# Performance work log

Measured on AMD Instinct MI355X. Metric: run time of the kernel, lower is better.

The kernel has to match this reference:

```python
import jax, jax.numpy as jnp
import numpy as np

BETA = 0.25  # commitment loss weight


def setup_inputs() -> dict:
    key = jax.random.key(0)
    k1, k2 = jax.random.split(key)
    N, K, d = 131072, 1024, 64
    z_e = jax.random.normal(k1, (N, d), dtype=jnp.float32)
    scale = 1.0 / np.sqrt(d)
    codebook = jax.random.uniform(k2, (K, d), minval=-scale, maxval=scale, dtype=jnp.float32)
    return {"z_e": z_e, "codebook": codebook}


def reference(z_e, codebook):
    d = codebook.shape[-1]
    flat = z_e.reshape(-1, d)                                  # (N, d)
    z_sq = jnp.sum(flat ** 2, axis=-1, keepdims=True)          # (N, 1)
    c_sq = jnp.sum(codebook ** 2, axis=-1)[None, :]            # (1, K)
    zc = flat @ codebook.T                                     # (N, K)
    dists = z_sq - 2.0 * zc + c_sq
    idx_flat = jnp.argmin(dists, axis=-1)                      # (N,)
    e_flat = codebook[idx_flat]                                # (N, d)
    z_q_flat_st = flat + jax.lax.stop_gradient(e_flat - flat)  # straight-through
    codebook_loss = jnp.mean((e_flat - jax.lax.stop_gradient(flat)) ** 2)
    commitment_loss = jnp.mean((jax.lax.stop_gradient(e_flat) - flat) ** 2)
    vq_loss = codebook_loss + BETA * commitment_loss
    indices = idx_flat.reshape(z_e.shape[:-1])
    z_q_st = z_q_flat_st.reshape(z_e.shape)
    return (indices, z_q_st, vq_loss)
```

## Files before the change

### kernel.cpp

```cpp
#include <hip/hip_runtime.h>
#include <stdint.h>

#define DIM 64
#define KC 1024
#define TILE 64
#define NT (KC / TILE)
#define TAU_HALF 5.0e-4f
#define FLAG_CAP 16384

typedef float f32x4 __attribute__((ext_vector_type(4)));
typedef short short8 __attribute__((ext_vector_type(8)));

__device__ __forceinline__ unsigned short bf16_rn(float f) {
  union { float f; uint32_t u; } v; v.f = f;
  uint32_t u = v.u;
  uint32_t r = u + 0x7fffu + ((u >> 16) & 1u);
  return (unsigned short)(r >> 16);
}
__device__ __forceinline__ float bf16_f32(unsigned short h) {
  union { uint32_t u; float f; } v; v.u = ((uint32_t)h) << 16;
  return v.f;
}
__device__ __forceinline__ void gll16(const void* g, void* l) {
  __builtin_amdgcn_global_load_lds(
      (const __attribute__((address_space(1))) void*)g,
      (__attribute__((address_space(3))) void*)l, 16, 0, 0);
}

__global__ void k1_prep(const float* __restrict__ cb,
                        unsigned short* __restrict__ cb_hi,
                        unsigned short* __restrict__ cb_lo,
                        float* __restrict__ csqh,
                        int* __restrict__ cnt) {
  const int k = blockIdx.x, j = threadIdx.x;
  const float c = cb[k * DIM + j];
  const unsigned short hi = bf16_rn(c);
  const float hif = bf16_f32(hi);
  const unsigned short lo = bf16_rn(c - hif);
  cb_hi[k * DIM + j] = hi;
  cb_lo[k * DIM + j] = lo;
  float s = c * c;
  #pragma unroll
  for (int off = 32; off >= 1; off >>= 1) s += __shfl_xor(s, off);
  if (j == 0) csqh[k] = -0.5f * s;
  if (k == 0 && j == 0) *cnt = 0;
}

__launch_bounds__(256, 4)
__global__ void k2_argmin(const float* __restrict__ z,
                          const unsigned short* __restrict__ cb_hi,
                          const unsigned short* __restrict__ cb_lo,
                          const float* __restrict__ csqh,
                          float* __restrict__ out_idx,
                          int* __restrict__ cnt,
                          int* __restrict__ flags,
                          float* __restrict__ partials) {
  __shared__ unsigned short lds_cb[2 * 8192];
  __shared__ float lds_csq[KC];

  const int tid  = threadIdx.x;
  const int lane = tid & 63;
  const int wv   = tid >> 6;
  const int wr   = wv >> 1;
  const int wc   = wv & 1;
  const int lg   = lane >> 4;
  const int lr   = lane & 15;
  const int row0 = blockIdx.x * 128;

  const unsigned short* gsrc[4];
  #pragma unroll
  for (int p = 0; p < 4; ++p) {
    const int cl = (p & 1) * 32 + wv * 8 + (lane >> 3);
    const int ch = (lane & 7) ^ (cl & 7);
    gsrc[p] = ((p >> 1) ? cb_lo : cb_hi) + cl * DIM + ch * 8;
  }

#define STAGE(tt, bs)                                                         \
  {                                                                           \
    const int _toff = (tt) * (TILE * DIM);                                    \
    _Pragma("unroll")                                                         \
    for (int p = 0; p < 4; ++p) {                                             \
      gll16(gsrc[p] + _toff,                                                  \
            (char*)lds_cb + (bs) * 16384 + (p * 256 + wv * 64) * 16);         \
    }                                                                         \
  }

  STAGE(0, 0);
  ((f32x4*)lds_csq)[tid] = ((const f32x4*)csqh)[tid];

  short8 zhi[4][2], zlo[4][2];
  float zsq[4];
  #pragma unroll
  for (int rt = 0; rt < 4; ++rt) {
    const int row = row0 + wr * 64 + rt * 16 + lr;
    float sq = 0.0f;
    #pragma unroll
    for (int ks = 0; ks < 2; ++ks) {
      const float* p = z + row * DIM + ks * 32 + lg * 8;
      const f32x4 va = *(const f32x4*)p;
      const f32x4 vb = *(const f32x4*)(p + 4);
      sq = fmaf(va[0], va[0], sq); sq = fmaf(va[1], va[1], sq);
      sq = fmaf(va[2], va[2], sq); sq = fmaf(va[3], va[3], sq);
      sq = fmaf(vb[0], vb[0], sq); sq = fmaf(vb[1], vb[1], sq);
      sq = fmaf(vb[2], vb[2], sq); sq = fmaf(vb[3], vb[3], sq);
      union { uint32_t w[4]; short8 s8; } H, L;
      #pragma unroll
      for (int pr = 0; pr < 4; ++pr) {
        const float f0 = (pr < 2) ? va[2 * pr]     : vb[2 * pr - 4];
        const float f1 = (pr < 2) ? va[2 * pr + 1] : vb[2 * pr - 3];
        const uint32_t u0 = __float_as_uint(f0);
        const uint32_t u1 = __float_as_uint(f1);
        H.w[pr] = __builtin_amdgcn_perm(u1, u0, 0x07060302u);
        const float l0 = f0 - __uint_as_float(u0 & 0xffff0000u);
        const float l1 = f1 - __uint_as_float(u1 & 0xffff0000u);
        uint32_t lw;
        asm("v_cvt_pk_bf16_f32 %0, %1, %2" : "=v"(lw) : "v"(l0), "v"(l1));
        L.w[pr] = lw;
      }
      zhi[rt][ks] = H.s8;
      zlo[rt][ks] = L.s8;
    }
    zsq[rt] = sq;
  }

  float M1[4], M2[4];
  int I1[4];
  #pragma unroll
  for (int rt = 0; rt < 4; ++rt) { M1[rt] = -3.0e38f; M2[rt] = -3.0e38f; I1[rt] = 0; }

  __syncthreads();

  for (int t = 0; t < NT; ++t) {
    if (t < NT - 1) STAGE(t + 1, (t + 1) & 1);
    const char* bufb = (const char*)lds_cb + (t & 1) * 16384;
    #pragma unroll
    for (int ct = 0; ct < 2; ++ct) {
      const int cbase = t * TILE + wc * 32 + ct * 16 + lg * 4;
      const f32x4 init = *(const f32x4*)&lds_csq[cbase];
      const int cl2 = wc * 32 + ct * 16 + lr;
      short8 cf[2][2];
      #pragma unroll
      for (int sp = 0; sp < 2; ++sp) {
        #pragma unroll
        for (int ks = 0; ks < 2; ++ks) {
          const int off = sp * 8192 + cl2 * 128 + (((ks * 4 + lg) ^ (cl2 & 7)) * 16);
          cf[sp][ks] = *(const short8*)(bufb + off);
        }
      }
      #pragma unroll
      for (int rt = 0; rt < 4; ++rt) {
        f32x4 acc = init;
        acc = __builtin_amdgcn_mfma_f32_16x16x32_bf16(cf[0][0], zhi[rt][0], acc, 0, 0, 0);
        acc = __builtin_amdgcn_mfma_f32_16x16x32_bf16(cf[0][1], zhi[rt][1], acc, 0, 0, 0);
        acc = __builtin_amdgcn_mfma_f32_16x16x32_bf16(cf[0][0], zlo[rt][0], acc, 0, 0, 0);
        acc = __builtin_amdgcn_mfma_f32_16x16x32_bf16(cf[0][1], zlo[rt][1], acc, 0, 0, 0);
        acc = __builtin_amdgcn_mfma_f32_16x16x32_bf16(cf[1][0], zhi[rt][0], acc, 0, 0, 0);
        acc = __builtin_amdgcn_mfma_f32_16x16x32_bf16(cf[1][1], zhi[rt][1], acc, 0, 0, 0);
        #pragma unroll
        for (int j = 0; j < 4; ++j) {
          const float s = acc[j];
          M2[rt] = __builtin_amdgcn_fmed3f(s, M1[rt], M2[rt]);
          const bool take = s > M1[rt];
          M1[rt] = fmaxf(s, M1[rt]);
          I1[rt] = take ? (cbase + j) : I1[rt];
        }
      }
    }
    __syncthreads();
  }

  float* S  = (float*)lds_cb;
  float* S2 = S + 256;
  int*   SI = (int*)(S + 512);
  float* ZS = (float*)(SI + 256);
  float* CT = ZS + 128;

  #pragma unroll
  for (int rt = 0; rt < 4; ++rt) {
    float m1 = M1[rt], m2 = M2[rt];
    int i1 = I1[rt];
    #pragma unroll
    for (int off = 16; off <= 32; off <<= 1) {
      const float o1 = __shfl_xor(m1, off);
      const float o2 = __shfl_xor(m2, off);
      const int   oi = __shfl_xor(i1, off);
      m2 = fmaxf(fmaxf(m2, o2), fminf(m1, o1));
      const bool take = (o1 > m1) || (o1 == m1 && oi < i1);
      if (take) { m1 = o1; i1 = oi; }
    }
    float zq = zsq[rt];
    zq += __shfl_xor(zq, 16);
    zq += __shfl_xor(zq, 32);
    if (lg == 0) {
      const int r = wr * 64 + rt * 16 + lr;
      S[wc * 128 + r]  = m1;
      S2[wc * 128 + r] = m2;
      SI[wc * 128 + r] = i1;
      if (wc == 0) ZS[r] = zq;
    }
  }
  __syncthreads();
  if (tid < 128) {
    const float a1 = S[tid],  b1 = S[128 + tid];
    const float a2 = S2[tid], b2 = S2[128 + tid];
    const int   ai = SI[tid], bi = SI[128 + tid];
    const bool takeB = (b1 > a1) || (b1 == a1 && bi < ai);
    const float m1 = takeB ? b1 : a1;
    const int  idx = takeB ? bi : ai;
    const float m2 = fmaxf(fmaxf(a2, b2), fminf(a1, b1));
    const int row = row0 + tid;
    out_idx[row] = (float)idx;
    CT[tid] = ZS[tid] - 2.0f * m1;
    if (m1 - m2 < TAU_HALF) {
      const int p = atomicAdd(cnt, 1);
      if (p < FLAG_CAP) flags[p] = row;
    }
  }
  __syncthreads();
  if (tid < 64) {
    float c = CT[tid] + CT[tid + 64];
    #pragma unroll
    for (int off = 32; off >= 1; off >>= 1) c += __shfl_xor(c, off);
    if (tid == 0) partials[blockIdx.x] = c;
  }
#undef STAGE
}

__global__ void k3_rescue(const float* __restrict__ z,
                          const float* __restrict__ cb,
                          const float* __restrict__ csqh,
                          float* __restrict__ out_idx,
                          const int* __restrict__ cnt,
                          const int* __restrict__ flags) {
  int n = *cnt;
  if (n > FLAG_CAP) n = FLAG_CAP;
  const int lane = threadIdx.x & 63;
  const int w = blockIdx.x * 4 + (threadIdx.x >> 6);
  for (int i = w; i < n; i += gridDim.x * 4) {
    const int row = flags[i];
    const f32x4* zr4 = (const f32x4*)(z + (size_t)row * DIM);
    float m1 = -3.0e38f;
    int i1 = 0;
    for (int kk = 0; kk < 16; ++kk) {
      const int k = lane * 16 + kk;
      const f32x4* cp = (const f32x4*)(cb + (size_t)k * DIM);
      float acc = csqh[k];
      #pragma unroll
      for (int j4 = 0; j4 < DIM / 4; ++j4) {
        const f32x4 c4 = cp[j4];
        const f32x4 z4 = zr4[j4];
        acc = fmaf(z4[0], c4[0], acc);
        acc = fmaf(z4[1], c4[1], acc);
        acc = fmaf(z4[2], c4[2], acc);
        acc = fmaf(z4[3], c4[3], acc);
      }
      if (acc > m1) { m1 = acc; i1 = k; }
    }
    #pragma unroll
    for (int off = 32; off >= 1; off >>= 1) {
      const float o1 = __shfl_xor(m1, off);
      const int   oi = __shfl_xor(i1, off);
      if (o1 > m1 || (o1 == m1 && oi < i1)) { m1 = o1; i1 = oi; }
    }
    if (lane == 0) out_idx[row] = (float)i1;
  }
}

__global__ void k4_scatter(const float* __restrict__ cb,
                           const float* __restrict__ out_idx,
                           float* __restrict__ zq) {
  const int gid = blockIdx.x * 256 + threadIdx.x;
  const int row = gid >> 2;
  const int q0  = (gid & 3) * 4;
  const int idx = (int)out_idx[row];
  const f32x4* src = (const f32x4*)(cb + (size_t)idx * DIM) + q0;
  f32x4* dst = (f32x4*)(zq + (size_t)row * DIM) + q0;
  dst[0] = src[0]; dst[1] = src[1]; dst[2] = src[2]; dst[3] = src[3];
}

__global__ void k5_reduce(const float* __restrict__ partials,
                          float* __restrict__ loss_slot,
                          float scale, int nb) {
  __shared__ float wsum[4];
  const int tid = threadIdx.x;
  float s = 0.0f;
  for (int i = tid; i < nb / 4; i += 256) {
    const f32x4 v = ((const f32x4*)partials)[i];
    s += (v[0] + v[1]) + (v[2] + v[3]);
  }
  #pragma unroll
  for (int off = 32; off >= 1; off >>= 1) s += __shfl_xor(s, off);
  if ((tid & 63) == 0) wsum[tid >> 6] = s;
  __syncthreads();
  if (tid == 0) *loss_slot = (wsum[0] + wsum[1] + wsum[2] + wsum[3]) * scale;
}

extern "C" void kernel_launch(void* const* d_in, const int* in_sizes, int n_in,
                              void* d_out, int out_size, void* d_ws, size_t ws_size,
                              hipStream_t stream) {
  const float* z  = (const float*)d_in[0];
  const float* cb = (const float*)d_in[1];
  const int N = in_sizes[0] / DIM;

  float* out       = (float*)d_out;
  float* out_idx   = out;
  float* zq        = out + N;
  float* loss_slot = out + N + (size_t)N * DIM;

  unsigned short* cb_hi = (unsigned short*)d_ws;
  unsigned short* cb_lo = cb_hi + KC * DIM;
  float* csqh = (float*)(cb_lo + KC * DIM);
  int* cnt    = (int*)(csqh + KC);
  int* flags  = cnt + 64;
  float* partials = (float*)(flags + FLAG_CAP);

  const int nb2 = N / 128;
  const float scale = 1.25f / ((float)N * (float)DIM);

  k1_prep<<<KC, DIM, 0, stream>>>(cb, cb_hi, cb_lo, csqh, cnt);
  k2_argmin<<<nb2, 256, 0, stream>>>(z, cb_hi, cb_lo, csqh, out_idx, cnt, flags, partials);
  k3_rescue<<<256, 256, 0, stream>>>(z, cb, csqh, out_idx, cnt, flags);
  k4_scatter<<<N / 64, 256, 0, stream>>>(cb, out_idx, zq);
  k5_reduce<<<1, 256, 0, stream>>>(partials, loss_slot, scale, nb2);
}
```

Baseline: 185.5 us.

## Hold full bf16 codebook in LDS, drop lo split, fuse scatter into argmin

Loads the whole codebook, as bf16 hi parts only, into LDS once per 1024-thread block of 512 rows, replacing the double-buffered tiled staging. It drops the codebook lo-part MFMAs (four MFMAs per tile instead of six) and widens the near-tie rescue threshold to compensate for the lower precision. The z_q gather is fused into the argmin and rescue kernels, which removes the separate scatter kernel. The risks are more rows flagged for the scalar rescue pass, whose flag capacity is raised, and lower occupancy from the 128KB+ LDS allocation.

```diff
diff --git a/kernel.cpp b/kernel.cpp
--- a/kernel.cpp
+++ b/kernel.cpp
@@ -3,10 +3,9 @@
 
 #define DIM 64
 #define KC 1024
-#define TILE 64
-#define NT (KC / TILE)
-#define TAU_HALF 5.0e-4f
-#define FLAG_CAP 16384
+#define ROWS_PER_BLOCK 512
+#define TAU 8.0e-3f
+#define FLAG_CAP 65536
 
 typedef float f32x4 __attribute__((ext_vector_type(4)));
 typedef short short8 __attribute__((ext_vector_type(8)));
@@ -17,10 +16,6 @@
   uint32_t r = u + 0x7fffu + ((u >> 16) & 1u);
   return (unsigned short)(r >> 16);
 }
-__device__ __forceinline__ float bf16_f32(unsigned short h) {
-  union { uint32_t u; float f; } v; v.u = ((uint32_t)h) << 16;
-  return v.f;
-}
 __device__ __forceinline__ void gll16(const void* g, void* l) {
   __builtin_amdgcn_global_load_lds(
       (const __attribute__((address_space(1))) void*)g,
@@ -29,16 +24,11 @@
 
 __global__ void k1_prep(const float* __restrict__ cb,
                         unsigned short* __restrict__ cb_hi,
-                        unsigned short* __restrict__ cb_lo,
                         float* __restrict__ csqh,
                         int* __restrict__ cnt) {
   const int k = blockIdx.x, j = threadIdx.x;
   const float c = cb[k * DIM + j];
-  const unsigned short hi = bf16_rn(c);
-  const float hif = bf16_f32(hi);
-  const unsigned short lo = bf16_rn(c - hif);
-  cb_hi[k * DIM + j] = hi;
-  cb_lo[k * DIM + j] = lo;
+  cb_hi[k * DIM + j] = bf16_rn(c);
   float s = c * c;
   #pragma unroll
   for (int off = 32; off >= 1; off >>= 1) s += __shfl_xor(s, off);
@@ -46,57 +36,45 @@
   if (k == 0 && j == 0) *cnt = 0;
 }
 
-__launch_bounds__(256, 4)
+__launch_bounds__(1024, 4)
 __global__ void k2_argmin(const float* __restrict__ z,
                           const unsigned short* __restrict__ cb_hi,
-                          const unsigned short* __restrict__ cb_lo,
                           const float* __restrict__ csqh,
+                          const float* __restrict__ cb,
                           float* __restrict__ out_idx,
+                          float* __restrict__ zq,
                           int* __restrict__ cnt,
                           int* __restrict__ flags,
                           float* __restrict__ partials) {
-  __shared__ unsigned short lds_cb[2 * 8192];
+  __shared__ unsigned short lds_cb[KC * DIM];
   __shared__ float lds_csq[KC];
+  __shared__ float wpart[16];
 
   const int tid  = threadIdx.x;
   const int lane = tid & 63;
   const int wv   = tid >> 6;
-  const int wr   = wv >> 1;
-  const int wc   = wv & 1;
   const int lg   = lane >> 4;
   const int lr   = lane & 15;
-  const int row0 = blockIdx.x * 128;
-
-  const unsigned short* gsrc[4];
-  #pragma unroll
-  for (int p = 0; p < 4; ++p) {
-    const int cl = (p & 1) * 32 + wv * 8 + (lane >> 3);
-    const int ch = (lane & 7) ^ (cl & 7);
-    gsrc[p] = ((p >> 1) ? cb_lo : cb_hi) + cl * DIM + ch * 8;
-  }
-
-#define STAGE(tt, bs)                                                         \
-  {                                                                           \
-    const int _toff = (tt) * (TILE * DIM);                                    \
-    _Pragma("unroll")                                                         \
-    for (int p = 0; p < 4; ++p) {                                             \
-      gll16(gsrc[p] + _toff,                                                  \
-            (char*)lds_cb + (bs) * 16384 + (p * 256 + wv * 64) * 16);         \
-    }                                                                         \
-  }
-
-  STAGE(0, 0);
-  ((f32x4*)lds_csq)[tid] = ((const f32x4*)csqh)[tid];
-
-  short8 zhi[4][2], zlo[4][2];
-  float zsq[4];
-  #pragma unroll
-  for (int rt = 0; rt < 4; ++rt) {
-    const int row = row0 + wr * 64 + rt * 16 + lr;
+  const int row0 = blockIdx.x * ROWS_PER_BLOCK;
+
+  #pragma unroll
+  for (int p = 0; p < 8; ++p) {
+    const int linear = p * 1024 + tid;
+    const int ch = linear & 7;
+    const int cl = linear >> 3;
+    gll16(cb_hi + cl * DIM + ((ch ^ (cl & 7)) * 8), (char*)lds_cb + linear * 16);
+  }
+  if (tid < KC / 4) ((f32x4*)lds_csq)[tid] = ((const f32x4*)csqh)[tid];
+
+  short8 zhi[2][2], zlo[2][2];
+  float zsq[2];
+  #pragma unroll
+  for (int rt = 0; rt < 2; ++rt) {
+    const int row = row0 + wv * 32 + rt * 16 + lr;
     float sq = 0.0f;
     #pragma unroll
     for (int ks = 0; ks < 2; ++ks) {
-      const float* p = z + row * DIM + ks * 32 + lg * 8;
+      const float* p = z + (size_t)row * DIM + ks * 32 + lg * 8;
       const f32x4 va = *(const f32x4*)p;
       const f32x4 vb = *(const f32x4*)(p + 4);
       sq = fmaf(va[0], va[0], sq); sq = fmaf(va[1], va[1], sq);
@@ -123,60 +101,43 @@
     zsq[rt] = sq;
   }
 
-  float M1[4], M2[4];
-  int I1[4];
-  #pragma unroll
-  for (int rt = 0; rt < 4; ++rt) { M1[rt] = -3.0e38f; M2[rt] = -3.0e38f; I1[rt] = 0; }
-
-  __syncthreads();
-
-  for (int t = 0; t < NT; ++t) {
-    if (t < NT - 1) STAGE(t + 1, (t + 1) & 1);
-    const char* bufb = (const char*)lds_cb + (t & 1) * 16384;
-    #pragma unroll
-    for (int ct = 0; ct < 2; ++ct) {
-      const int cbase = t * TILE + wc * 32 + ct * 16 + lg * 4;
-      const f32x4 init = *(const f32x4*)&lds_csq[cbase];
-      const int cl2 = wc * 32 + ct * 16 + lr;
-      short8 cf[2][2];
+  float M1[2] = {-3.0e38f, -3.0e38f}, M2[2] = {-3.0e38f, -3.0e38f};
+  int I1[2] = {0, 0};
+
+  __syncthreads();
+
+  const int off0 = lr * 128 + ((lg)     ^ (lr & 7)) * 16;
+  const int off1 = lr * 128 + ((4 + lg) ^ (lr & 7)) * 16;
+
+  #pragma unroll 2
+  for (int ct = 0; ct < KC / 16; ++ct) {
+    const int cbase = ct * 16 + lg * 4;
+    const f32x4 init = *(const f32x4*)&lds_csq[cbase];
+    const char* base = (const char*)lds_cb + ct * 2048;
+    const short8 cf0 = *(const short8*)(base + off0);
+    const short8 cf1 = *(const short8*)(base + off1);
+    #pragma unroll
+    for (int rt = 0; rt < 2; ++rt) {
+      f32x4 acc = init;
+      acc = __builtin_amdgcn_mfma_f32_16x16x32_bf16(cf0, zhi[rt][0], acc, 0, 0, 0);
+      acc = __builtin_amdgcn_mfma_f32_16x16x32_bf16(cf1, zhi[rt][1], acc, 0, 0, 0);
+      acc = __builtin_amdgcn_mfma_f32_16x16x32_bf16(cf0, zlo[rt][0], acc, 0, 0, 0);
+      acc = __builtin_amdgcn_mfma_f32_16x16x32_bf16(cf1, zlo[rt][1], acc, 0, 0, 0);
       #pragma unroll
-      for (int sp = 0; sp < 2; ++sp) {
-        #pragma unroll
-        for (int ks = 0; ks < 2; ++ks) {
-          const int off = sp * 8192 + cl2 * 128 + (((ks * 4 + lg) ^ (cl2 & 7)) * 16);
-          cf[sp][ks] = *(const short8*)(bufb + off);
-        }
-      }
-      #pragma unroll
-      for (int rt = 0; rt < 4; ++rt) {
-        f32x4 acc = init;
-        acc = __builtin_amdgcn_mfma_f32_16x16x32_bf16(cf[0][0], zhi[rt][0], acc, 0, 0, 0);
-        acc = __builtin_amdgcn_mfma_f32_16x16x32_bf16(cf[0][1], zhi[rt][1], acc, 0, 0, 0);
-        acc = __builtin_amdgcn_mfma_f32_16x16x32_bf16(cf[0][0], zlo[rt][0], acc, 0, 0, 0);
-        acc = __builtin_amdgcn_mfma_f32_16x16x32_bf16(cf[0][1], zlo[rt][1], acc, 0, 0, 0);
-        acc = __builtin_amdgcn_mfma_f32_16x16x32_bf16(cf[1][0], zhi[rt][0], acc, 0, 0, 0);
-        acc = __builtin_amdgcn_mfma_f32_16x16x32_bf16(cf[1][1], zhi[rt][1], acc, 0, 0, 0);
-        #pragma unroll
-        for (int j = 0; j < 4; ++j) {
-          const float s = acc[j];
-          M2[rt] = __builtin_amdgcn_fmed3f(s, M1[rt], M2[rt]);
-          const bool take = s > M1[rt];
-          M1[rt] = fmaxf(s, M1[rt]);
-          I1[rt] = take ? (cbase + j) : I1[rt];
-        }
-      }
-    }
-    __syncthreads();
-  }
-
-  float* S  = (float*)lds_cb;
-  float* S2 = S + 256;
-  int*   SI = (int*)(S + 512);
-  float* ZS = (float*)(SI + 256);
-  float* CT = ZS + 128;
-
-  #pragma unroll
-  for (int rt = 0; rt < 4; ++rt) {
+      for (int j = 0; j < 4; ++j) {
+        const float s = acc[j];
+        M2[rt] = __builtin_amdgcn_fmed3f(s, M1[rt], M2[rt]);
+        const bool take = s > M1[rt];
+        M1[rt] = fmaxf(s, M1[rt]);
+        I1[rt] = take ? (cbase + j) : I1[rt];
+      }
+    }
+  }
+
+  float M1b[2], M2b[2], loss01 = 0.0f;
+  int idxr[2];
+  #pragma unroll
+  for (int rt = 0; rt < 2; ++rt) {
     float m1 = M1[rt], m2 = M2[rt];
     int i1 = I1[rt];
     #pragma unroll
@@ -188,48 +149,53 @@
       const bool take = (o1 > m1) || (o1 == m1 && oi < i1);
       if (take) { m1 = o1; i1 = oi; }
     }
-    float zq = zsq[rt];
-    zq += __shfl_xor(zq, 16);
-    zq += __shfl_xor(zq, 32);
-    if (lg == 0) {
-      const int r = wr * 64 + rt * 16 + lr;
-      S[wc * 128 + r]  = m1;
-      S2[wc * 128 + r] = m2;
-      SI[wc * 128 + r] = i1;
-      if (wc == 0) ZS[r] = zq;
-    }
-  }
-  __syncthreads();
-  if (tid < 128) {
-    const float a1 = S[tid],  b1 = S[128 + tid];
-    const float a2 = S2[tid], b2 = S2[128 + tid];
-    const int   ai = SI[tid], bi = SI[128 + tid];
-    const bool takeB = (b1 > a1) || (b1 == a1 && bi < ai);
-    const float m1 = takeB ? b1 : a1;
-    const int  idx = takeB ? bi : ai;
-    const float m2 = fmaxf(fmaxf(a2, b2), fminf(a1, b1));
-    const int row = row0 + tid;
-    out_idx[row] = (float)idx;
-    CT[tid] = ZS[tid] - 2.0f * m1;
-    if (m1 - m2 < TAU_HALF) {
-      const int p = atomicAdd(cnt, 1);
-      if (p < FLAG_CAP) flags[p] = row;
-    }
-  }
-  __syncthreads();
-  if (tid < 64) {
-    float c = CT[tid] + CT[tid + 64];
-    #pragma unroll
-    for (int off = 32; off >= 1; off >>= 1) c += __shfl_xor(c, off);
-    if (tid == 0) partials[blockIdx.x] = c;
-  }
-#undef STAGE
+    float zs = zsq[rt];
+    zs += __shfl_xor(zs, 16);
+    zs += __shfl_xor(zs, 32);
+    M1b[rt] = m1; M2b[rt] = m2; idxr[rt] = i1;
+    loss01 += zs - 2.0f * m1;
+  }
+
+  __syncthreads();
+  int* idxL = (int*)lds_csq;
+  if (lane < 16) {
+    #pragma unroll
+    for (int rt = 0; rt < 2; ++rt) {
+      const int r = wv * 32 + rt * 16 + lr;
+      out_idx[row0 + r] = (float)idxr[rt];
+      idxL[r] = idxr[rt];
+      if (M1b[rt] - M2b[rt] < TAU) {
+        const int p = atomicAdd(cnt, 1);
+        if (p < FLAG_CAP) flags[p] = row0 + r;
+      }
+    }
+  }
+  float lsum = loss01;
+  #pragma unroll
+  for (int off = 1; off <= 32; off <<= 1) lsum += __shfl_xor(lsum, off);
+  if (lane == 0) wpart[wv] = lsum * 0.25f;
+  __syncthreads();
+  if (tid == 0) {
+    float s = 0.0f;
+    #pragma unroll
+    for (int i = 0; i < 16; ++i) s += wpart[i];
+    partials[blockIdx.x] = s;
+  }
+  {
+    const int r2 = tid >> 1, half = tid & 1;
+    const int idx = idxL[r2];
+    const f32x4* src = (const f32x4*)(cb + (size_t)idx * DIM + half * 32);
+    f32x4* dst = (f32x4*)(zq + (size_t)(row0 + r2) * DIM + half * 32);
+    dst[0] = src[0];
+    dst[1] = src[1];
+  }
 }
 
 __global__ void k3_rescue(const float* __restrict__ z,
                           const float* __restrict__ cb,
                           const float* __restrict__ csqh,
                           float* __restrict__ out_idx,
+                          float* __restrict__ zq,
                           const int* __restrict__ cnt,
                           const int* __restrict__ flags) {
   int n = *cnt;
@@ -263,19 +229,10 @@
       if (o1 > m1 || (o1 == m1 && oi < i1)) { m1 = o1; i1 = oi; }
     }
     if (lane == 0) out_idx[row] = (float)i1;
-  }
-}
-
-__global__ void k4_scatter(const float* __restrict__ cb,
-                           const float* __restrict__ out_idx,
-                           float* __restrict__ zq) {
-  const int gid = blockIdx.x * 256 + threadIdx.x;
-  const int row = gid >> 2;
-  const int q0  = (gid & 3) * 4;
-  const int idx = (int)out_idx[row];
-  const f32x4* src = (const f32x4*)(cb + (size_t)idx * DIM) + q0;
-  f32x4* dst = (f32x4*)(zq + (size_t)row * DIM) + q0;
-  dst[0] = src[0]; dst[1] = src[1]; dst[2] = src[2]; dst[3] = src[3];
+    if (lane < 16)
+      ((f32x4*)(zq + (size_t)row * DIM))[lane] =
+          ((const f32x4*)(cb + (size_t)i1 * DIM))[lane];
+  }
 }
 
 __global__ void k5_reduce(const float* __restrict__ partials,
@@ -308,18 +265,16 @@
   float* loss_slot = out + N + (size_t)N * DIM;
 
   unsigned short* cb_hi = (unsigned short*)d_ws;
-  unsigned short* cb_lo = cb_hi + KC * DIM;
-  float* csqh = (float*)(cb_lo + KC * DIM);
+  float* csqh = (float*)(cb_hi + KC * DIM);
   int* cnt    = (int*)(csqh + KC);
-  int* flags  = cnt + 64;
-  float* partials = (float*)(flags + FLAG_CAP);
-
-  const int nb2 = N / 128;
+  float* partials = (float*)(cnt + 64);
+  int* flags  = (int*)(partials + 256);
+
+  const int nb2 = N / ROWS_PER_BLOCK;
   const float scale = 1.25f / ((float)N * (float)DIM);
 
-  k1_prep<<<KC, DIM, 0, stream>>>(cb, cb_hi, cb_lo, csqh, cnt);
-  k2_argmin<<<nb2, 256, 0, stream>>>(z, cb_hi, cb_lo, csqh, out_idx, cnt, flags, partials);
-  k3_rescue<<<256, 256, 0, stream>>>(z, cb, csqh, out_idx, cnt, flags);
-  k4_scatter<<<N / 64, 256, 0, stream>>>(cb, out_idx, zq);
+  k1_prep<<<KC, DIM, 0, stream>>>(cb, cb_hi, csqh, cnt);
+  k2_argmin<<<nb2, 1024, 0, stream>>>(z, cb_hi, csqh, cb, out_idx, zq, cnt, flags, partials);
+  k3_rescue<<<256, 256, 0, stream>>>(z, cb, csqh, out_idx, zq, cnt, flags);
   k5_reduce<<<1, 256, 0, stream>>>(partials, loss_slot, scale, nb2);
 }
```

Result: slower. 386.7 us (+108.5%).
